# Kernel tuning notes

Measured on AMD Instinct MI355X. Metric: run time of the kernel, lower is better.

## Reference

```python
import jax, jax.numpy as jnp
import numpy as np
from jax import lax

B = 16
C = 80                      # num_classes
IMG = 1024                  # square input image (H = W)
STRIDES = (8, 16, 32, 64, 128)
FEAT = (128, 64, 32, 16, 8) # IMG / stride per FPN level
SCORE_THRESH = 0.2
NMS_THRESH = 0.6
TOPK = 1000                 # topk_candidates per level
DETS = 100                  # detections_per_img


def _make_anchors(fs, stride):
    # one anchor per location, width = height = stride, centered on the cell
    ys, xs = jnp.meshgrid(jnp.arange(fs, dtype=jnp.float32),
                          jnp.arange(fs, dtype=jnp.float32), indexing="ij")
    cx = (xs.reshape(-1) + 0.5) * stride
    cy = (ys.reshape(-1) + 0.5) * stride
    h = stride / 2.0
    return jnp.stack([cx - h, cy - h, cx + h, cy + h], axis=-1)


def setup_inputs() -> dict:
    key = jax.random.key(0)
    ks = jax.random.split(key, 15)
    inp = {}
    for l, (fs, st) in enumerate(zip(FEAT, STRIDES)):
        hw = fs * fs
        inp[f"cls{l}"] = jax.random.normal(ks[3 * l + 0], (B, hw, C), jnp.float32)
        inp[f"ctr{l}"] = jax.random.normal(ks[3 * l + 1], (B, hw, 1), jnp.float32)
        inp[f"reg{l}"] = jax.random.uniform(ks[3 * l + 2], (B, hw, 4), jnp.float32)
        inp[f"anc{l}"] = _make_anchors(fs, st)
    return inp


def _decode(rel, anc):
    # BoxLinearCoder.decode with normalize_by_size=True
    cx = (anc[..., 0] + anc[..., 2]) * 0.5
    cy = (anc[..., 1] + anc[..., 3]) * 0.5
    w = anc[..., 2] - anc[..., 0]
    h = anc[..., 3] - anc[..., 1]
    rel = rel * jnp.stack([w, h, w, h], axis=-1)
    return jnp.stack([cx - rel[..., 0], cy - rel[..., 1],
                      cx + rel[..., 2], cy + rel[..., 3]], axis=-1)


def _level_candidates(cls, ctr, reg, anc):
    # score = sqrt(sigmoid(cls) * sigmoid(ctrness)), per torchvision FCOS
    scores = jnp.sqrt(jax.nn.sigmoid(cls) * jax.nn.sigmoid(ctr))  # [B,HW,C]
    flat = scores.reshape(scores.shape[0], -1)                    # [B,HW*C]
    # emulate the score threshold with masking (invalid -> -1, sorts last)
    masked = jnp.where(flat > SCORE_THRESH, flat, -1.0)
    k = min(TOPK, flat.shape[1])
    top_s, top_i = lax.top_k(masked, k)                           # [B,k]
    a_idx = top_i // C
    labels = top_i % C
    reg_sel = jnp.take_along_axis(reg, a_idx[..., None], axis=1)  # [B,k,4]
    boxes = _decode(reg_sel, anc[a_idx])                          # [B,k,4]
    boxes = jnp.clip(boxes, 0.0, float(IMG))                      # clip to image
    return boxes, top_s, labels


def _nms_single(boxes, scores, labels):
    # class-batched greedy NMS on one image, fixed DETS output slots
    off = jnp.float32(IMG + 1)
    nb = boxes + (labels.astype(boxes.dtype) * off)[:, None]  # class offset trick
    areas = (nb[:, 2] - nb[:, 0]) * (nb[:, 3] - nb[:, 1])

    def body(i, carry):
        s, bo, so, lo = carry
        j = jnp.argmax(s)
        bo = bo.at[i].set(boxes[j])
        so = so.at[i].set(s[j])
        lo = lo.at[i].set(labels[j])
        bj = nb[j]
        xx1 = jnp.maximum(bj[0], nb[:, 0])
        yy1 = jnp.maximum(bj[1], nb[:, 1])
        xx2 = jnp.minimum(bj[2], nb[:, 2])
        yy2 = jnp.minimum(bj[3], nb[:, 3])
        inter = jnp.maximum(xx2 - xx1, 0.0) * jnp.maximum(yy2 - yy1, 0.0)
        iou = inter / (areas + areas[j] - inter + 1e-9)
        s = jnp.where(iou > NMS_THRESH, -jnp.inf, s)  # suppress (incl. j itself)
        return s, bo, so, lo

    init = (scores,
            jnp.zeros((DETS, 4), boxes.dtype),
            jnp.zeros((DETS,), scores.dtype),
            jnp.zeros((DETS,), labels.dtype))
    _, bo, so, lo = lax.fori_loop(0, DETS, body, init)
    valid = so > SCORE_THRESH
    bo = jnp.where(valid[:, None], bo, 0.0)
    so = jnp.where(valid, so, 0.0)
    lo = jnp.where(valid, lo, -1)
    return bo, so, lo


def reference(cls0, cls1, cls2, cls3, cls4,
              ctr0, ctr1, ctr2, ctr3, ctr4,
              reg0, reg1, reg2, reg3, reg4,
              anc0, anc1, anc2, anc3, anc4):
    clss = (cls0, cls1, cls2, cls3, cls4)
    ctrs = (ctr0, ctr1, ctr2, ctr3, ctr4)
    regs = (reg0, reg1, reg2, reg3, reg4)
    ancs = (anc0, anc1, anc2, anc3, anc4)
    all_b, all_s, all_l = [], [], []
    for cls, ctr, reg, anc in zip(clss, ctrs, regs, ancs):
        b, s, l = _level_candidates(cls, ctr, reg, anc)
        all_b.append(b); all_s.append(s); all_l.append(l)
    boxes = jnp.concatenate(all_b, axis=1)    # [B, sum_k, 4]
    scores = jnp.concatenate(all_s, axis=1)   # [B, sum_k]
    labels = jnp.concatenate(all_l, axis=1)   # [B, sum_k]
    return jax.vmap(_nms_single)(boxes, scores, labels)
```

## Files before the change

### kernel.cpp

```cpp
#include <hip/hip_runtime.h>
#include <stdint.h>

namespace {

constexpr int kB = 16;
constexpr int kC = 80;
constexpr int kNLev = 5;
constexpr int kTopK = 1000;
constexpr int kDets = 100;
constexpr int kNBins = 512;
constexpr int kCap = 6144;
constexpr float kScoreT = 0.2f;
constexpr float kNmsT = 0.6f;
constexpr int kChunk = 16384;
constexpr int kNTot = kNLev * kTopK;
constexpr int kChunksPerImg = 108;
constexpr int kLvlChunk0[5] = {0, 80, 100, 105, 107};
constexpr int kLvlNChunk[5] = {80, 20, 5, 2, 1};

struct LvlPtrs {
  const float* reg[5];
  const float* anc[5];
};

struct ClsPtrs {
  const float* cls[5];
  const float* ctr[5];
};

__device__ __forceinline__ float sigm(float x) {
  return 1.0f / (1.0f + expf(-x));
}
__device__ __forceinline__ float sigm_fast(float x) {
  return __builtin_amdgcn_rcpf(1.0f + __expf(-x));
}

__device__ __forceinline__ void chunk_map(int c, int* L, int* ch) {
  if (c < 80)       { *L = 0; *ch = c; }
  else if (c < 100) { *L = 1; *ch = c - 80; }
  else if (c < 105) { *L = 2; *ch = c - 100; }
  else if (c < 107) { *L = 3; *ch = c - 105; }
  else              { *L = 4; *ch = 0; }
}

__global__ void __launch_bounds__(256)
khist_all(ClsPtrs CP, unsigned int* __restrict__ ph) {
  const int b = blockIdx.x / kChunksPerImg;
  const int c = blockIdx.x % kChunksPerImg;
  int L, ch; chunk_map(c, &L, &ch);
  const int HW = 16384 >> (2 * L);
  const int N = HW * kC;
  const int start = ch * kChunk;
  const int end = (start + kChunk < N) ? (start + kChunk) : N;
  __shared__ unsigned int lh[kNBins];
  for (int i = threadIdx.x; i < kNBins; i += 256) lh[i] = 0;
  __syncthreads();
  const float* clsb = CP.cls[L] + (size_t)b * N;
  const float* ctrb = CP.ctr[L] + (size_t)b * HW;
  const int tid4 = (int)threadIdx.x * 4;
#pragma unroll 1
  for (int bb = 0; bb < 2; ++bb) {
    const int base = start + bb * 8192;
    float4 vf[8]; int ke[8]; bool kv[8];
#pragma unroll
    for (int k = 0; k < 8; ++k) {
      int e = base + k * 1024 + tid4;
      ke[k] = e; kv[k] = (e < end);
      if (kv[k]) vf[k] = *reinterpret_cast<const float4*>(clsb + e);
    }
#pragma unroll
    for (int k = 0; k < 8; ++k) {
      if (!kv[k]) continue;
      const int e = ke[k];
      const int loc0 = (int)((unsigned)e / 80u);
      const int c0 = e - loc0 * kC;
      int loc1 = loc0 + 1; if (loc1 >= HW) loc1 = HW - 1;
      const float st0 = sigm_fast(ctrb[loc0]);
      const float st1 = sigm_fast(ctrb[loc1]);
      const float f[4] = {vf[k].x, vf[k].y, vf[k].z, vf[k].w};
#pragma unroll
      for (int q = 0; q < 4; ++q) {
        float st = (c0 + q >= kC) ? st1 : st0;
        float sc = __builtin_amdgcn_sqrtf(sigm_fast(f[q]) * st);
        int bin = (int)((sc - kScoreT) * 640.0f);
        if (bin >= 0) {
          if (bin > kNBins - 1) bin = kNBins - 1;
          atomicAdd(&lh[bin], 1u);
        }
      }
    }
  }
  __syncthreads();
  unsigned int* dst = ph + (size_t)blockIdx.x * kNBins;
  for (int i = threadIdx.x; i < kNBins; i += 256) dst[i] = lh[i];
}

__global__ void __launch_bounds__(256)
kcutoff(const unsigned int* __restrict__ ph, int* __restrict__ cutoff) {
  const int g = blockIdx.x;
  const int b = g / kNLev, L = g % kNLev;
  const unsigned int* base =
      ph + (size_t)(b * kChunksPerImg + kLvlChunk0[L]) * kNBins;
  const int nb = kLvlNChunk[L];
  __shared__ unsigned int lh[kNBins];
  unsigned int a0 = 0, a1 = 0;
  for (int j = 0; j < nb; ++j) {
    a0 += base[(size_t)j * kNBins + threadIdx.x];
    a1 += base[(size_t)j * kNBins + 256 + threadIdx.x];
  }
  lh[threadIdx.x] = a0;
  lh[256 + threadIdx.x] = a1;
  __syncthreads();
  if (threadIdx.x == 0) {
    unsigned int acc = 0; int cut = 0;
    for (int bin = kNBins - 1; bin >= 0; --bin) {
      acc += lh[bin];
      if (acc >= (unsigned)kTopK) { cut = bin; break; }
    }
    cutoff[g] = cut;
  }
}

__global__ void __launch_bounds__(256)
kcompact_all(ClsPtrs CP, const int* __restrict__ cutoff, unsigned int* __restrict__ cnt,
             unsigned long long* __restrict__ cand) {
  const int b = blockIdx.x / kChunksPerImg;
  const int c = blockIdx.x % kChunksPerImg;
  int L, ch; chunk_map(c, &L, &ch);
  const int HW = 16384 >> (2 * L);
  const int N = HW * kC;
  const int start = ch * kChunk;
  const int end = (start + kChunk < N) ? (start + kChunk) : N;
  const int g = b * kNLev + L;
  float thr = kScoreT + (float)(cutoff[g] - 2) * (1.0f / 640.0f);
  if (thr < 0.199f) thr = 0.199f;
  const float* clsb = CP.cls[L] + (size_t)b * N;
  const float* ctrb = CP.ctr[L] + (size_t)b * HW;
  unsigned long long* gc = cand + (size_t)g * kCap;
  const int tid4 = (int)threadIdx.x * 4;
#pragma unroll 1
  for (int bb = 0; bb < 2; ++bb) {
    const int base = start + bb * 8192;
    float4 vf[8]; int ke[8]; bool kv[8];
#pragma unroll
    for (int k = 0; k < 8; ++k) {
      int e = base + k * 1024 + tid4;
      ke[k] = e; kv[k] = (e < end);
      if (kv[k]) vf[k] = *reinterpret_cast<const float4*>(clsb + e);
    }
#pragma unroll
    for (int k = 0; k < 8; ++k) {
      if (!kv[k]) continue;
      const int e = ke[k];
      const int loc0 = (int)((unsigned)e / 80u);
      const int c0 = e - loc0 * kC;
      int loc1 = loc0 + 1; if (loc1 >= HW) loc1 = HW - 1;
      const float t0 = ctrb[loc0];
      const float t1 = ctrb[loc1];
      const float st0 = sigm_fast(t0);
      const float st1 = sigm_fast(t1);
      const float f[4] = {vf[k].x, vf[k].y, vf[k].z, vf[k].w};
#pragma unroll
      for (int q = 0; q < 4; ++q) {
        const bool hi = (c0 + q >= kC);
        float st = hi ? st1 : st0;
        float sa = __builtin_amdgcn_sqrtf(sigm_fast(f[q]) * st);
        if (sa >= thr) {
          float traw = hi ? t1 : t0;
          float sex = sqrtf(sigm(f[q]) * sigm(traw));
          if (sex > kScoreT) {
            unsigned int slot = atomicAdd(&cnt[g], 1u);
            if (slot < (unsigned)kCap) {
              int ee = e + q;
              unsigned int inv = 0xFFFFFFu - (((unsigned)L << 21) | (unsigned)ee);
              gc[slot] = ((unsigned long long)__float_as_uint(sex) << 24) | inv;
            }
          }
        }
      }
    }
  }
}

__global__ void __launch_bounds__(1024)
krankl(const unsigned long long* __restrict__ cand, const unsigned int* __restrict__ cnt,
       unsigned long long* __restrict__ lvlsorted) {
  const int g = blockIdx.x;
  const int l = g % kNLev;
  __shared__ unsigned long long s[kCap];
  unsigned int nu = cnt[g];
  const int n = (nu > (unsigned)kCap) ? kCap : (int)nu;
  for (int i = threadIdx.x; i < n; i += 1024)
    s[i] = cand[(size_t)g * kCap + i];
  __syncthreads();
  for (int p = n + (int)threadIdx.x; p < kTopK; p += 1024)
    lvlsorted[(size_t)g * kTopK + p] =
        (unsigned long long)(kNTot - (l * kTopK + p));
  for (int i = threadIdx.x; i < n; i += 1024) {
    const unsigned long long ki = s[i];
    int r = 0;
#pragma unroll 8
    for (int j = 0; j < n; ++j) r += (s[j] > ki) ? 1 : 0;
    if (r < kTopK) lvlsorted[(size_t)g * kTopK + r] = ki;
  }
}

__device__ __forceinline__ void decode_key(unsigned long long key, int b, const LvlPtrs& P,
                                           float4* box, int* label_out, float* score_out) {
  float sc = __uint_as_float((unsigned int)(key >> 24));
  *score_out = sc;
  if (!(sc > kScoreT)) { *box = make_float4(0.f, 0.f, 0.f, 0.f); *label_out = -1; return; }
  unsigned int pk = 0xFFFFFFu - (unsigned int)(key & 0xFFFFFFu);
  int l = pk >> 21;
  int idx = pk & 0x1FFFFF;
  int pos = idx / kC;
  int label = idx - pos * kC;
  int hw = 16384 >> (2 * l);
  const float* rg = P.reg[l] + ((size_t)b * hw + pos) * 4;
  const float* an = P.anc[l] + (size_t)pos * 4;
  float a0 = an[0], a1 = an[1], a2 = an[2], a3 = an[3];
  float cx = (a0 + a2) * 0.5f, cy = (a1 + a3) * 0.5f;
  float w = a2 - a0, h = a3 - a1;
  float x0 = cx - rg[0] * w, y0 = cy - rg[1] * h;
  float x1 = cx + rg[2] * w, y1 = cy + rg[3] * h;
  x0 = fminf(fmaxf(x0, 0.f), 1024.f);
  y0 = fminf(fmaxf(y0, 0.f), 1024.f);
  x1 = fminf(fmaxf(x1, 0.f), 1024.f);
  y1 = fminf(fmaxf(y1, 0.f), 1024.f);
  *box = make_float4(x0, y0, x1, y1);
  *label_out = label;
}

__global__ void krank(const unsigned long long* __restrict__ lvlsorted,
                      unsigned long long* __restrict__ skey,
                      float4* __restrict__ obox, LvlPtrs P) {
  int gid = blockIdx.x * blockDim.x + threadIdx.x;
  if (gid >= kB * kNTot) return;
  int b = gid / kNTot;
  int r0 = gid - b * kNTot;
  int a = r0 / kTopK, p = r0 - a * kTopK;
  const unsigned long long* base = lvlsorted + (size_t)b * kNTot;
  unsigned long long key = base[a * kTopK + p];
  int rank = p;
  for (int a2 = 0; a2 < kNLev; ++a2) {
    if (a2 == a) continue;
    const unsigned long long* lst = base + a2 * kTopK;
    int lo = 0, hi = kTopK;
    while (lo < hi) {
      int mid = (lo + hi) >> 1;
      if (lst[mid] > key) lo = mid + 1; else hi = mid;
    }
    rank += lo;
  }
  float4 box; int label; float sc;
  decode_key(key, b, P, &box, &label, &sc);
  float off = (sc > kScoreT) ? (float)label * 1025.0f : 0.0f;
  skey[(size_t)b * kNTot + rank] = key;
  obox[(size_t)b * kNTot + rank] =
      make_float4(box.x + off, box.y + off, box.z + off, box.w + off);
}

__global__ void __launch_bounds__(64)
knms(const unsigned long long* __restrict__ skey, const float4* __restrict__ obox,
     LvlPtrs P, float* __restrict__ out) {
  const int b = blockIdx.x;
  const int lane = threadIdx.x;
  __shared__ float4 kbox[kDets];
  __shared__ float karea[kDets];
  __shared__ unsigned long long kkey[kDets];
  const unsigned long long* keys = skey + (size_t)b * kNTot;
  const float4* boxes = obox + (size_t)b * kNTot;
  int nkept = 0;
  for (int base = 0; base < kNTot && nkept < kDets; base += 64) {
    int j = base + lane;
    unsigned long long key = (j < kNTot) ? keys[j] : 0ull;
    float sc = __uint_as_float((unsigned int)(key >> 24));
    bool scval = (j < kNTot) && (sc > kScoreT);
    if (__ballot(scval) == 0ull) break;
    float4 bx = make_float4(0.f, 0.f, 0.f, 0.f);
    if (scval) bx = boxes[j];
    float area = (bx.z - bx.x) * (bx.w - bx.y);
    bool alive = scval;
    for (int k = 0; k < nkept; ++k) {
      float4 kb = kbox[k];
      float xx1 = fmaxf(kb.x, bx.x), yy1 = fmaxf(kb.y, bx.y);
      float xx2 = fminf(kb.z, bx.z), yy2 = fminf(kb.w, bx.w);
      float inter = fmaxf(xx2 - xx1, 0.f) * fmaxf(yy2 - yy1, 0.f);
      float iou = inter / (area + karea[k] - inter + 1e-9f);
      if (iou > kNmsT) alive = false;
    }
    unsigned long long mask = __ballot(alive);
    while (mask != 0ull && nkept < kDets) {
      int lead = (int)__builtin_ctzll(mask);
      float lx = __shfl(bx.x, lead);
      float ly = __shfl(bx.y, lead);
      float lz = __shfl(bx.z, lead);
      float lw = __shfl(bx.w, lead);
      float la = __shfl(area, lead);
      unsigned int khi = (unsigned int)__shfl((int)(key >> 32), lead);
      unsigned int klo = (unsigned int)__shfl((int)(key & 0xFFFFFFFFull), lead);
      if (lane == 0) {
        kbox[nkept] = make_float4(lx, ly, lz, lw);
        karea[nkept] = la;
        kkey[nkept] = (((unsigned long long)khi) << 32) | (unsigned long long)klo;
      }
      __syncthreads();
      ++nkept;
      float xx1 = fmaxf(lx, bx.x), yy1 = fmaxf(ly, bx.y);
      float xx2 = fminf(lz, bx.z), yy2 = fminf(lw, bx.w);
      float inter = fmaxf(xx2 - xx1, 0.f) * fmaxf(yy2 - yy1, 0.f);
      float iou = inter / (area + la - inter + 1e-9f);
      if (iou > kNmsT) alive = false;
      mask = __ballot(alive);
    }
  }
  for (int s = lane; s < kDets; s += 64) {
    float4 bo = make_float4(0.f, 0.f, 0.f, 0.f);
    float so = 0.f, lo = -1.f;
    if (s < nkept) {
      float4 box; int label; float sc;
      decode_key(kkey[s], b, P, &box, &label, &sc);
      bo = box; so = sc; lo = (float)label;
    }
    size_t bi = (size_t)b * kDets + s;
    out[bi * 4 + 0] = bo.x;
    out[bi * 4 + 1] = bo.y;
    out[bi * 4 + 2] = bo.z;
    out[bi * 4 + 3] = bo.w;
    out[(size_t)kB * kDets * 4 + bi] = so;
    out[(size_t)kB * kDets * 5 + bi] = lo;
  }
}

}

extern "C" void kernel_launch(void* const* d_in, const int* in_sizes, int n_in,
                              void* d_out, int out_size, void* d_ws, size_t ws_size,
                              hipStream_t stream) {
  ClsPtrs CP; LvlPtrs P;
  for (int l = 0; l < 5; ++l) {
    CP.cls[l] = (const float*)d_in[4 * l + 0];
    CP.ctr[l] = (const float*)d_in[4 * l + 1];
    P.reg[l]  = (const float*)d_in[4 * l + 2];
    P.anc[l]  = (const float*)d_in[4 * l + 3];
  }

  const int nblk = kB * kChunksPerImg;

  char* w = (char*)d_ws;
  unsigned int* ph = (unsigned int*)w;            w += (size_t)nblk * kNBins * 4;
  int* cutoff = (int*)w;                          w += 80 * 4;
  unsigned int* cnt = (unsigned int*)w;           w += 80 * 4;
  unsigned long long* cand = (unsigned long long*)w;      w += (size_t)80 * kCap * 8;
  unsigned long long* lvlsorted = (unsigned long long*)w; w += (size_t)80 * kTopK * 8;
  unsigned long long* skeyp = (unsigned long long*)w;     w += (size_t)kB * kNTot * 8;
  float4* oboxp = (float4*)w;                     w += (size_t)kB * kNTot * 16;

  hipMemsetAsync(cutoff, 0, 80 * 8, stream);

  khist_all<<<nblk, 256, 0, stream>>>(CP, ph);

  kcutoff<<<80, 256, 0, stream>>>(ph, cutoff);

  kcompact_all<<<nblk, 256, 0, stream>>>(CP, cutoff, cnt, cand);

  krankl<<<80, 1024, 0, stream>>>(cand, cnt, lvlsorted);

  int rblocks = (kB * kNTot + 255) / 256;
  krank<<<rblocks, 256, 0, stream>>>(lvlsorted, skeyp, oboxp, P);

  knms<<<kB, 64, 0, stream>>>(skeyp, oboxp, P, (float*)d_out);
}
```

Before: 276.7 us.

## Halve chunk size, merge histograms via global atomics, move exact rescoring to separate kernel

Each block now processes 8192 elements instead of 16384, doubling the grid to 214 chunks per image for more parallelism. Per-block histograms are atomically merged into one histogram per image-level, so kcutoff no longer has to sum many partial histograms. The compact kernel now writes only candidate indices after the fast-math filter, and a new krescore kernel recomputes the exact sigmoid score for each candidate. This moves the precise expf work off the hot streaming pass, at the cost of an extra launch, a gather of cls and ctr values, and the global atomics on the histogram.

```diff
diff --git a/kernel.cpp b/kernel.cpp
--- a/kernel.cpp
+++ b/kernel.cpp
@@ -12,11 +12,9 @@
 constexpr int kCap = 6144;
 constexpr float kScoreT = 0.2f;
 constexpr float kNmsT = 0.6f;
-constexpr int kChunk = 16384;
+constexpr int kChunk = 8192;
 constexpr int kNTot = kNLev * kTopK;
-constexpr int kChunksPerImg = 108;
-constexpr int kLvlChunk0[5] = {0, 80, 100, 105, 107};
-constexpr int kLvlNChunk[5] = {80, 20, 5, 2, 1};
+constexpr int kChunksPerImg = 214;
 
 struct LvlPtrs {
   const float* reg[5];
@@ -36,15 +34,15 @@
 }
 
 __device__ __forceinline__ void chunk_map(int c, int* L, int* ch) {
-  if (c < 80)       { *L = 0; *ch = c; }
-  else if (c < 100) { *L = 1; *ch = c - 80; }
-  else if (c < 105) { *L = 2; *ch = c - 100; }
-  else if (c < 107) { *L = 3; *ch = c - 105; }
+  if (c < 160)      { *L = 0; *ch = c; }
+  else if (c < 200) { *L = 1; *ch = c - 160; }
+  else if (c < 210) { *L = 2; *ch = c - 200; }
+  else if (c < 213) { *L = 3; *ch = c - 210; }
   else              { *L = 4; *ch = 0; }
 }
 
 __global__ void __launch_bounds__(256)
-khist_all(ClsPtrs CP, unsigned int* __restrict__ ph) {
+khist_all(ClsPtrs CP, unsigned int* __restrict__ ghist) {
   const int b = blockIdx.x / kChunksPerImg;
   const int c = blockIdx.x % kChunksPerImg;
   int L, ch; chunk_map(c, &L, &ch);
@@ -58,58 +56,48 @@
   const float* clsb = CP.cls[L] + (size_t)b * N;
   const float* ctrb = CP.ctr[L] + (size_t)b * HW;
   const int tid4 = (int)threadIdx.x * 4;
-#pragma unroll 1
-  for (int bb = 0; bb < 2; ++bb) {
-    const int base = start + bb * 8192;
-    float4 vf[8]; int ke[8]; bool kv[8];
-#pragma unroll
-    for (int k = 0; k < 8; ++k) {
-      int e = base + k * 1024 + tid4;
-      ke[k] = e; kv[k] = (e < end);
-      if (kv[k]) vf[k] = *reinterpret_cast<const float4*>(clsb + e);
-    }
-#pragma unroll
-    for (int k = 0; k < 8; ++k) {
-      if (!kv[k]) continue;
-      const int e = ke[k];
-      const int loc0 = (int)((unsigned)e / 80u);
-      const int c0 = e - loc0 * kC;
-      int loc1 = loc0 + 1; if (loc1 >= HW) loc1 = HW - 1;
-      const float st0 = sigm_fast(ctrb[loc0]);
-      const float st1 = sigm_fast(ctrb[loc1]);
-      const float f[4] = {vf[k].x, vf[k].y, vf[k].z, vf[k].w};
-#pragma unroll
-      for (int q = 0; q < 4; ++q) {
-        float st = (c0 + q >= kC) ? st1 : st0;
-        float sc = __builtin_amdgcn_sqrtf(sigm_fast(f[q]) * st);
-        int bin = (int)((sc - kScoreT) * 640.0f);
-        if (bin >= 0) {
-          if (bin > kNBins - 1) bin = kNBins - 1;
-          atomicAdd(&lh[bin], 1u);
-        }
+  float4 vf[8]; int ke[8]; bool kv[8];
+#pragma unroll
+  for (int k = 0; k < 8; ++k) {
+    int e = start + k * 1024 + tid4;
+    ke[k] = e; kv[k] = (e < end);
+    if (kv[k]) vf[k] = *reinterpret_cast<const float4*>(clsb + e);
+  }
+#pragma unroll
+  for (int k = 0; k < 8; ++k) {
+    if (!kv[k]) continue;
+    const int e = ke[k];
+    const int loc0 = (int)((unsigned)e / 80u);
+    const int c0 = e - loc0 * kC;
+    int loc1 = loc0 + 1; if (loc1 >= HW) loc1 = HW - 1;
+    const float st0 = sigm_fast(ctrb[loc0]);
+    const float st1 = sigm_fast(ctrb[loc1]);
+    const float f[4] = {vf[k].x, vf[k].y, vf[k].z, vf[k].w};
+#pragma unroll
+    for (int q = 0; q < 4; ++q) {
+      float st = (c0 + q >= kC) ? st1 : st0;
+      float sc = __builtin_amdgcn_sqrtf(sigm_fast(f[q]) * st);
+      int bin = (int)((sc - kScoreT) * 640.0f);
+      if (bin >= 0) {
+        if (bin > kNBins - 1) bin = kNBins - 1;
+        atomicAdd(&lh[bin], 1u);
       }
     }
   }
   __syncthreads();
-  unsigned int* dst = ph + (size_t)blockIdx.x * kNBins;
-  for (int i = threadIdx.x; i < kNBins; i += 256) dst[i] = lh[i];
+  const int g = b * kNLev + L;
+  unsigned int* gh = ghist + (size_t)g * kNBins;
+  for (int i = threadIdx.x; i < kNBins; i += 256)
+    if (lh[i]) atomicAdd(&gh[i], lh[i]);
 }
 
 __global__ void __launch_bounds__(256)
-kcutoff(const unsigned int* __restrict__ ph, int* __restrict__ cutoff) {
+kcutoff(const unsigned int* __restrict__ ghist, int* __restrict__ cutoff) {
   const int g = blockIdx.x;
-  const int b = g / kNLev, L = g % kNLev;
-  const unsigned int* base =
-      ph + (size_t)(b * kChunksPerImg + kLvlChunk0[L]) * kNBins;
-  const int nb = kLvlNChunk[L];
+  const unsigned int* h = ghist + (size_t)g * kNBins;
   __shared__ unsigned int lh[kNBins];
-  unsigned int a0 = 0, a1 = 0;
-  for (int j = 0; j < nb; ++j) {
-    a0 += base[(size_t)j * kNBins + threadIdx.x];
-    a1 += base[(size_t)j * kNBins + 256 + threadIdx.x];
-  }
-  lh[threadIdx.x] = a0;
-  lh[256 + threadIdx.x] = a1;
+  lh[threadIdx.x] = h[threadIdx.x];
+  lh[256 + threadIdx.x] = h[256 + threadIdx.x];
   __syncthreads();
   if (threadIdx.x == 0) {
     unsigned int acc = 0; int cut = 0;
@@ -123,7 +111,7 @@
 
 __global__ void __launch_bounds__(256)
 kcompact_all(ClsPtrs CP, const int* __restrict__ cutoff, unsigned int* __restrict__ cnt,
-             unsigned long long* __restrict__ cand) {
+             unsigned int* __restrict__ candidx) {
   const int b = blockIdx.x / kChunksPerImg;
   const int c = blockIdx.x % kChunksPerImg;
   int L, ch; chunk_map(c, &L, &ch);
@@ -136,50 +124,57 @@
   if (thr < 0.199f) thr = 0.199f;
   const float* clsb = CP.cls[L] + (size_t)b * N;
   const float* ctrb = CP.ctr[L] + (size_t)b * HW;
-  unsigned long long* gc = cand + (size_t)g * kCap;
+  unsigned int* gi = candidx + (size_t)g * kCap;
   const int tid4 = (int)threadIdx.x * 4;
-#pragma unroll 1
-  for (int bb = 0; bb < 2; ++bb) {
-    const int base = start + bb * 8192;
-    float4 vf[8]; int ke[8]; bool kv[8];
-#pragma unroll
-    for (int k = 0; k < 8; ++k) {
-      int e = base + k * 1024 + tid4;
-      ke[k] = e; kv[k] = (e < end);
-      if (kv[k]) vf[k] = *reinterpret_cast<const float4*>(clsb + e);
-    }
-#pragma unroll
-    for (int k = 0; k < 8; ++k) {
-      if (!kv[k]) continue;
-      const int e = ke[k];
-      const int loc0 = (int)((unsigned)e / 80u);
-      const int c0 = e - loc0 * kC;
-      int loc1 = loc0 + 1; if (loc1 >= HW) loc1 = HW - 1;
-      const float t0 = ctrb[loc0];
-      const float t1 = ctrb[loc1];
-      const float st0 = sigm_fast(t0);
-      const float st1 = sigm_fast(t1);
-      const float f[4] = {vf[k].x, vf[k].y, vf[k].z, vf[k].w};
-#pragma unroll
-      for (int q = 0; q < 4; ++q) {
-        const bool hi = (c0 + q >= kC);
-        float st = hi ? st1 : st0;
-        float sa = __builtin_amdgcn_sqrtf(sigm_fast(f[q]) * st);
-        if (sa >= thr) {
-          float traw = hi ? t1 : t0;
-          float sex = sqrtf(sigm(f[q]) * sigm(traw));
-          if (sex > kScoreT) {
-            unsigned int slot = atomicAdd(&cnt[g], 1u);
-            if (slot < (unsigned)kCap) {
-              int ee = e + q;
-              unsigned int inv = 0xFFFFFFu - (((unsigned)L << 21) | (unsigned)ee);
-              gc[slot] = ((unsigned long long)__float_as_uint(sex) << 24) | inv;
-            }
-          }
-        }
+  float4 vf[8]; int ke[8]; bool kv[8];
+#pragma unroll
+  for (int k = 0; k < 8; ++k) {
+    int e = start + k * 1024 + tid4;
+    ke[k] = e; kv[k] = (e < end);
+    if (kv[k]) vf[k] = *reinterpret_cast<const float4*>(clsb + e);
+  }
+#pragma unroll
+  for (int k = 0; k < 8; ++k) {
+    if (!kv[k]) continue;
+    const int e = ke[k];
+    const int loc0 = (int)((unsigned)e / 80u);
+    const int c0 = e - loc0 * kC;
+    int loc1 = loc0 + 1; if (loc1 >= HW) loc1 = HW - 1;
+    const float st0 = sigm_fast(ctrb[loc0]);
+    const float st1 = sigm_fast(ctrb[loc1]);
+    const float f[4] = {vf[k].x, vf[k].y, vf[k].z, vf[k].w};
+#pragma unroll
+    for (int q = 0; q < 4; ++q) {
+      float st = (c0 + q >= kC) ? st1 : st0;
+      float sa = __builtin_amdgcn_sqrtf(sigm_fast(f[q]) * st);
+      if (sa >= thr) {
+        unsigned int slot = atomicAdd(&cnt[g], 1u);
+        if (slot < (unsigned)kCap) gi[slot] = (unsigned int)(e + q);
       }
     }
   }
+}
+
+__global__ void __launch_bounds__(256)
+krescore(ClsPtrs CP, const unsigned int* __restrict__ cnt,
+         const unsigned int* __restrict__ candidx,
+         unsigned long long* __restrict__ cand) {
+  const int gid = blockIdx.x * 256 + (int)threadIdx.x;
+  const int g = gid / kCap;
+  const int slot = gid - g * kCap;
+  if (g >= kB * kNLev) return;
+  unsigned int n = cnt[g]; if (n > (unsigned)kCap) n = kCap;
+  if (slot >= (int)n) return;
+  const unsigned int e = candidx[(size_t)g * kCap + slot];
+  const int b = g / kNLev, L = g - (g / kNLev) * kNLev;
+  const int HW = 16384 >> (2 * L);
+  const int loc = (int)(e / 80u);
+  const float cv = CP.cls[L][(size_t)b * HW * kC + e];
+  const float tv = CP.ctr[L][(size_t)b * HW + loc];
+  const float sex = sqrtf(sigm(cv) * sigm(tv));
+  const unsigned int inv = 0xFFFFFFu - (((unsigned)L << 21) | e);
+  cand[(size_t)g * kCap + slot] =
+      ((unsigned long long)__float_as_uint(sex) << 24) | inv;
 }
 
 __global__ void __launch_bounds__(1024)
@@ -348,21 +343,24 @@
   const int nblk = kB * kChunksPerImg;
 
   char* w = (char*)d_ws;
-  unsigned int* ph = (unsigned int*)w;            w += (size_t)nblk * kNBins * 4;
+  unsigned int* hist = (unsigned int*)w;          w += (size_t)80 * kNBins * 4;
   int* cutoff = (int*)w;                          w += 80 * 4;
   unsigned int* cnt = (unsigned int*)w;           w += 80 * 4;
+  unsigned int* candidx = (unsigned int*)w;       w += (size_t)80 * kCap * 4;
   unsigned long long* cand = (unsigned long long*)w;      w += (size_t)80 * kCap * 8;
   unsigned long long* lvlsorted = (unsigned long long*)w; w += (size_t)80 * kTopK * 8;
   unsigned long long* skeyp = (unsigned long long*)w;     w += (size_t)kB * kNTot * 8;
   float4* oboxp = (float4*)w;                     w += (size_t)kB * kNTot * 16;
 
-  hipMemsetAsync(cutoff, 0, 80 * 8, stream);
-
-  khist_all<<<nblk, 256, 0, stream>>>(CP, ph);
-
-  kcutoff<<<80, 256, 0, stream>>>(ph, cutoff);
-
-  kcompact_all<<<nblk, 256, 0, stream>>>(CP, cutoff, cnt, cand);
+  hipMemsetAsync(hist, 0, (size_t)80 * kNBins * 4 + 80 * 8, stream);
+
+  khist_all<<<nblk, 256, 0, stream>>>(CP, hist);
+
+  kcutoff<<<80, 256, 0, stream>>>(hist, cutoff);
+
+  kcompact_all<<<nblk, 256, 0, stream>>>(CP, cutoff, cnt, candidx);
+
+  krescore<<<(80 * kCap) / 256, 256, 0, stream>>>(CP, cnt, candidx, cand);
 
   krankl<<<80, 1024, 0, stream>>>(cand, cnt, lvlsorted);
 
```

After: 347.6 us. 25.6% more time.
